# Optimization experiments

Measured on AMD Instinct MI355X. Metric: run time of the kernel, lower is better.

Reference implementation:

```python
import jax, jax.numpy as jnp
import numpy as np

HEADS = 16  # init kwarg 'heads'

def setup_inputs() -> dict:
    key = jax.random.key(0)
    k1, k2, k3 = jax.random.split(key, 3)
    B, S, D = 2, 2048, 1024
    x = jax.random.normal(k1, (B, S, D), dtype=jnp.float32)
    # nn.Linear(dim, 3*dim, bias=False): y = x @ W^T; store as [D, 3D] already transposed.
    w_qkv = jax.random.normal(k2, (D, 3 * D), dtype=jnp.float32) * 0.02
    w_out = jax.random.normal(k3, (D, D), dtype=jnp.float32) * 0.02
    return {"x": x, "w_qkv": w_qkv, "w_out": w_out}

def reference(x, w_qkv, w_out):
    B, S, D = x.shape
    H = HEADS
    hd = D // H
    scale = 1.0 / jnp.sqrt(jnp.asarray(hd, dtype=x.dtype))
    qkv = x @ w_qkv                      # [B, S, 3D]
    q, k, v = jnp.split(qkv, 3, axis=-1)
    def to_heads(t):
        return t.reshape(B, S, H, hd).transpose(0, 2, 1, 3)  # [B, H, S, hd]
    q, k, v = to_heads(q), to_heads(k), to_heads(v)
    scores = jnp.einsum('bhqd,bhkd->bhqk', q, k) * scale      # [B, H, S, S]
    # causal mask: query i attends to keys j <= i
    causal = jnp.tril(jnp.ones((S, S), dtype=bool))
    scores = jnp.where(causal, scores, -jnp.inf)
    p = jax.nn.softmax(scores, axis=-1)  # online-softmax in the original == exact softmax
    o = jnp.einsum('bhqk,bhkd->bhqd', p, v)                   # [B, H, S, hd]
    out = o.transpose(0, 2, 1, 3).reshape(B, S, D)
    return out @ w_out
```

## Files before the change

kernel.cpp:

```cpp
#include <hip/hip_runtime.h>


typedef unsigned short u16;
typedef unsigned int   u32;
typedef __attribute__((ext_vector_type(4))) u16    u16x4;
typedef __attribute__((ext_vector_type(8))) u16    u16x8;
typedef __attribute__((ext_vector_type(4))) short  s16x4;
typedef __attribute__((ext_vector_type(8))) __bf16 bf16x8;
typedef __attribute__((ext_vector_type(4))) float  f32x4;
typedef __attribute__((ext_vector_type(16))) float f32x16;

#define DEV static __device__ __forceinline__

DEV u16 f2b(float f) {
  unsigned u = __float_as_uint(f);
  u += 0x7fffu + ((u >> 16) & 1u);
  return (u16)(u >> 16);
}

DEV void gload_lds16(const void* g, void* l) {
  __builtin_amdgcn_global_load_lds((const __attribute__((address_space(1))) void*)g,
                                   (__attribute__((address_space(3))) void*)l, 16, 0, 0);
}

DEV unsigned lds_off(const void* p) {
  return (unsigned)(unsigned long long)(const __attribute__((address_space(3))) void*)p;
}

DEV s16x4 tr_read(unsigned off) {
  s16x4 d;
  asm volatile("ds_read_b64_tr_b16 %0, %1" : "=v"(d) : "v"(off));
  return d;
}

DEV u32 cvt_pk(float lo, float hi) {
  u32 r;
  asm("v_cvt_pk_bf16_f32 %0, %1, %2" : "=v"(r) : "v"(lo), "v"(hi));
  return r;
}

DEV void pswap(u32& x, u32& y) {
  asm volatile("v_permlane32_swap_b32 %0, %1" : "+v"(x), "+v"(y));
}

DEV f32x4 mfma32(bf16x8 a, bf16x8 b, f32x4 c) {
  return __builtin_amdgcn_mfma_f32_16x16x32_bf16(a, b, c, 0, 0, 0);
}
DEV f32x16 mfma3232(bf16x8 a, bf16x8 b, f32x16 c) {
  return __builtin_amdgcn_mfma_f32_32x32x16_bf16(a, b, c, 0, 0, 0);
}

__global__ __launch_bounds__(256) void prep_kernel(const float* __restrict__ x,
                                                   u16* __restrict__ xb,
                                                   const float* __restrict__ w_qkv,
                                                   u16* __restrict__ wqkvT,
                                                   const float* __restrict__ w_out,
                                                   u16* __restrict__ woutT) {
  __shared__ u16 ls[32][33];
  const int bid = (int)blockIdx.x;
  const int t = threadIdx.x;
  if (bid < 4096) {
    const int i = bid * 256 + t;
    const float4 v = ((const float4*)x)[i];
    u16x4 o = { f2b(v.x), f2b(v.y), f2b(v.z), f2b(v.w) };
    ((u16x4*)xb)[i] = o;
    return;
  }
  const float* w; u16* wt; int Ndim, tn, tk; float s;
  if (bid < 7168) {
    const int q = bid - 4096;
    w = w_qkv; wt = wqkvT; Ndim = 3072;
    tn = (q % 96) * 32; tk = (q / 96) * 32;
    s = (tn < 1024) ? 0.18033688011112042f : 1.0f;
  } else {
    const int q = bid - 7168;
    w = w_out; wt = woutT; Ndim = 1024;
    tn = (q % 32) * 32; tk = (q / 32) * 32;
    s = 1.0f;
  }
  const int r = t >> 3, c4 = (t & 7) * 4;
  const float4 v = *(const float4*)(w + (size_t)(tk + r) * Ndim + tn + c4);
  ls[r][c4 + 0] = f2b(v.x * s); ls[r][c4 + 1] = f2b(v.y * s);
  ls[r][c4 + 2] = f2b(v.z * s); ls[r][c4 + 3] = f2b(v.w * s);
  __syncthreads();
  u16x4 ov = { ls[c4 + 0][r], ls[c4 + 1][r], ls[c4 + 2][r], ls[c4 + 3][r] };
  *(u16x4*)(wt + (size_t)(tn + r) * 1024 + tk + c4) = ov;
}

__global__ __launch_bounds__(512, 2) void gemm_qkv(const u16* __restrict__ A,
                                                   const u16* __restrict__ Bt,
                                                   u16* __restrict__ C, const int ldc) {
  const int gx = gridDim.x;
  const int id = (int)(blockIdx.y * gx + blockIdx.x);
  const int nxp = gx >> 3;
  const int xcd = id & 7, loc = id >> 3;
  const int tn = (xcd * nxp + loc % nxp) * 128;
  const int tm = (loc / nxp) * 128;
  const int tid = (int)threadIdx.x;
  const int lane = tid & 63, wid = tid >> 6;
  const int wm = wid >> 2, wn = wid & 3;
  const int lg = lane >> 4, lc = lane & 15;
  __shared__ __align__(128) u16 lsA[128 * 64];
  __shared__ __align__(128) u16 lsB[128 * 64];

  f32x4 acc[4][2];
#pragma unroll
  for (int i = 0; i < 4; ++i)
#pragma unroll
    for (int j = 0; j < 2; ++j) acc[i][j] = (f32x4){0.f, 0.f, 0.f, 0.f};

  for (int kt = 0; kt < 16; ++kt) {
#pragma unroll
    for (int c = 0; c < 2; ++c) {
      const int p = tid + c * 512;
      const int row = p >> 3, ck = p & 7;
      const int cg = ck ^ (row & 7);
      gload_lds16(A  + (size_t)(tm + row) * 1024 + kt * 64 + cg * 8, (char*)lsA + p * 16);
      gload_lds16(Bt + (size_t)(tn + row) * 1024 + kt * 64 + cg * 8, (char*)lsB + p * 16);
    }
    __syncthreads();
#pragma unroll
    for (int kk = 0; kk < 2; ++kk) {
      bf16x8 af[4], bg[2];
#pragma unroll
      for (int i = 0; i < 4; ++i) {
        const int ar = wm * 64 + i * 16 + lc;
        af[i] = *(const bf16x8*)(lsA + ar * 64 + ((kk * 4 + lg) ^ (ar & 7)) * 8);
      }
#pragma unroll
      for (int j = 0; j < 2; ++j) {
        const int br = wn * 32 + j * 16 + lc;
        bg[j] = *(const bf16x8*)(lsB + br * 64 + ((kk * 4 + lg) ^ (br & 7)) * 8);
      }
#pragma unroll
      for (int i = 0; i < 4; ++i)
#pragma unroll
        for (int j = 0; j < 2; ++j)
          acc[i][j] = mfma32(af[i], bg[j], acc[i][j]);
    }
    __syncthreads();
  }

#pragma unroll
  for (int i = 0; i < 4; ++i) {
#pragma unroll
    for (int r = 0; r < 4; ++r) {
      const int m = tm + wm * 64 + i * 16 + lg * 4 + r;
#pragma unroll
      for (int j = 0; j < 2; ++j) {
        const int n = tn + wn * 32 + j * 16 + lc;
        C[(size_t)m * ldc + n] = f2b(acc[i][j][r]);
      }
    }
  }
}

__global__ __launch_bounds__(256) void gemm_bt64(const u16* __restrict__ A,
                                                 const u16* __restrict__ Bt,
                                                 float* __restrict__ C, const int ldc) {
  const int id = (int)(blockIdx.y * 8 + blockIdx.x);
  const int tn = (id & 7) * 128;
  const int tm = (id >> 3) * 64;
  const int tid = threadIdx.x;
  const int wave = tid >> 6, lane = tid & 63;
  const int wc = wave;
  const int lg = lane >> 4, lc = lane & 15;
  __shared__ __align__(128) u16 lsA[64 * 32];
  __shared__ __align__(128) u16 lsB[128 * 32];

  f32x4 acc[4][2];
#pragma unroll
  for (int i = 0; i < 4; ++i)
#pragma unroll
    for (int j = 0; j < 2; ++j) acc[i][j] = (f32x4){0.f, 0.f, 0.f, 0.f};

  for (int kt = 0; kt < 32; ++kt) {
    {
      const int p = tid;
      const int row = p >> 2, ck = p & 3;
      const int cg = ck ^ ((row >> 1) & 3);
      gload_lds16(A + (size_t)(tm + row) * 1024 + kt * 32 + cg * 8, (char*)lsA + p * 16);
    }
#pragma unroll
    for (int c = 0; c < 2; ++c) {
      const int p = tid + c * 256;
      const int row = p >> 2, ck = p & 3;
      const int cg = ck ^ ((row >> 1) & 3);
      gload_lds16(Bt + (size_t)(tn + row) * 1024 + kt * 32 + cg * 8, (char*)lsB + p * 16);
    }
    __syncthreads();
    bf16x8 af[4], bg[2];
#pragma unroll
    for (int i = 0; i < 4; ++i) {
      const int ar = i * 16 + lc;
      af[i] = *(const bf16x8*)(lsA + ar * 32 + (lg ^ ((ar >> 1) & 3)) * 8);
    }
#pragma unroll
    for (int j = 0; j < 2; ++j) {
      const int br = wc * 32 + j * 16 + lc;
      bg[j] = *(const bf16x8*)(lsB + br * 32 + (lg ^ ((br >> 1) & 3)) * 8);
    }
#pragma unroll
    for (int i = 0; i < 4; ++i)
#pragma unroll
      for (int j = 0; j < 2; ++j)
        acc[i][j] = mfma32(af[i], bg[j], acc[i][j]);
    __syncthreads();
  }

#pragma unroll
  for (int i = 0; i < 4; ++i) {
#pragma unroll
    for (int r = 0; r < 4; ++r) {
      const int m = tm + i * 16 + lg * 4 + r;
#pragma unroll
      for (int j = 0; j < 2; ++j) {
        const int n = tn + wc * 32 + j * 16 + lc;
        C[(size_t)m * ldc + n] = acc[i][j][r];
      }
    }
  }
}

__global__ __launch_bounds__(256, 2) void attn_kernel(const u16* __restrict__ qkv,
                                                      u16* __restrict__ o) {
  const int qb  = 63 - (int)(blockIdx.x >> 5);
  const int bh  = blockIdx.x & 31;
  const int b   = bh >> 4, h = bh & 15;
  const int tid  = threadIdx.x;
  const int wave = tid >> 6, lane = tid & 63;
  const int l31 = lane & 31, lg2 = lane >> 5;

  __shared__ __align__(128) char smem[4][8192];
  __shared__ float lsm[4][32];
  char* wb = smem[wave];
  const unsigned vb = lds_off(wb + 4096);

  const size_t bS = (size_t)b * 2048;
  const int T  = qb + 1;
  const int q0 = qb * 32;

  const u16* qrow = qkv + (bS + q0 + l31) * 3072 + h * 64;
  bf16x8 qf[4];
#pragma unroll
  for (int m = 0; m < 4; ++m)
    qf[m] = *(const bf16x8*)(qrow + 16 * m + 8 * lg2);

  unsigned koff[4], voff[4];
#pragma unroll
  for (int c = 0; c < 4; ++c) {
    const int p = c * 64 + lane;
    {
      const int row = p >> 3;
      const int cg = (p & 7) ^ (row & 7);
      koff[c] = (unsigned)(row * 3072 + 1024 + h * 64 + cg * 8);
    }
    {
      const int s = p >> 3, cw = p & 7;
      voff[c] = (unsigned)((4 * (s >> 2) + (cw >> 1)) * 3072 + 2048 + h * 64
                           + (s & 3) * 16 + (cw & 1) * 8);
    }
  }

  auto STAGE = [&](int t) {
    const u16* base = qkv + (bS + (size_t)t * 32) * 3072;
#pragma unroll
    for (int c = 0; c < 4; ++c)
      gload_lds16(base + koff[c], wb + (c * 64 + lane) * 16);
#pragma unroll
    for (int c = 0; c < 4; ++c)
      gload_lds16(base + voff[c], wb + 4096 + (c * 64 + lane) * 16);
  };

  float lsum = 0.f;
  f32x16 accO[2];
#pragma unroll
  for (int r = 0; r < 16; ++r) { accO[0][r] = 0.f; accO[1][r] = 0.f; }

  if (wave < T) STAGE(wave);

  for (int t = wave; t < T; t += 4) {
    asm volatile("s_waitcnt vmcnt(0)" ::: "memory");
    __builtin_amdgcn_sched_barrier(0);

    const u16* kbp = (const u16*)wb + l31 * 64;
    bf16x8 kf[4];
#pragma unroll
    for (int m = 0; m < 4; ++m)
      kf[m] = *(const bf16x8*)(kbp + (((2 * m + lg2) ^ (l31 & 7)) * 8));
    s16x4 vr[2][2][2];
#pragma unroll
    for (int db = 0; db < 2; ++db)
#pragma unroll
      for (int hh = 0; hh < 2; ++hh) {
        const unsigned a0 = vb +
          (unsigned)(((4 * hh + 2 * lg2) * 4 + db * 2 + (l31 >> 4)) * 128 + (l31 & 15) * 8);
        vr[db][hh][0] = tr_read(a0);
        vr[db][hh][1] = tr_read(a0 + 512);
      }
    asm volatile("s_waitcnt lgkmcnt(0)" ::: "memory");
    __builtin_amdgcn_sched_barrier(0);

    if (t + 4 < T) STAGE(t + 4);
    __builtin_amdgcn_sched_barrier(0);

    f32x16 sc;
#pragma unroll
    for (int r = 0; r < 16; ++r) sc[r] = 0.f;
    __builtin_amdgcn_s_setprio(1);
#pragma unroll
    for (int m = 0; m < 4; ++m)
      sc = mfma3232(kf[m], qf[m], sc);
    __builtin_amdgcn_s_setprio(0);

    float pp[16];
    if (t == T - 1) {
#pragma unroll
      for (int r = 0; r < 16; ++r) {
        const int kvp = (r & 3) + 8 * (r >> 2) + 4 * lg2;
        pp[r] = (kvp <= l31) ? exp2f(sc[r]) : 0.f;
      }
    } else {
#pragma unroll
      for (int r = 0; r < 16; ++r) pp[r] = exp2f(sc[r]);
    }
#pragma unroll
    for (int r = 0; r < 16; ++r) lsum += pp[r];

    u32 a01 = cvt_pk(pp[0], pp[1]),   a23 = cvt_pk(pp[2], pp[3]);
    u32 b01 = cvt_pk(pp[4], pp[5]),   b23 = cvt_pk(pp[6], pp[7]);
    u32 c01 = cvt_pk(pp[8], pp[9]),   c23 = cvt_pk(pp[10], pp[11]);
    u32 d01 = cvt_pk(pp[12], pp[13]), d23 = cvt_pk(pp[14], pp[15]);
    pswap(a01, b01); pswap(a23, b23);
    pswap(c01, d01); pswap(c23, d23);
    union Frag { u32 w[4]; bf16x8 v; };
    Frag f0, f1;
    f0.w[0] = a01; f0.w[1] = a23; f0.w[2] = b01; f0.w[3] = b23;
    f1.w[0] = c01; f1.w[1] = c23; f1.w[2] = d01; f1.w[3] = d23;

    __builtin_amdgcn_s_setprio(1);
#pragma unroll
    for (int db = 0; db < 2; ++db) {
      union { s16x4 hh[2]; bf16x8 v; } u0, u1;
      u0.hh[0] = vr[db][0][0]; u0.hh[1] = vr[db][0][1];
      u1.hh[0] = vr[db][1][0]; u1.hh[1] = vr[db][1][1];
      accO[db] = mfma3232(f0.v, u0.v, accO[db]);
      accO[db] = mfma3232(f1.v, u1.v, accO[db]);
    }
    __builtin_amdgcn_s_setprio(0);
  }

  lsum += __shfl_xor(lsum, 32);
  if (lane < 32) lsm[wave][l31] = lsum;
  float* mA = (float*)smem[0];
  float* mB = (float*)smem[2];
  __syncthreads();
  if ((wave & 1) == 0) {
    float* m = (wave == 0) ? mA : mB;
#pragma unroll
    for (int db = 0; db < 2; ++db)
#pragma unroll
      for (int r = 0; r < 16; ++r) {
        const int qp = (r & 3) + 8 * (r >> 2) + 4 * lg2;
        m[qp * 64 + db * 32 + l31] = accO[db][r];
      }
  }
  __syncthreads();
  if ((wave & 1) == 1) {
    float* m = (wave == 1) ? mA : mB;
#pragma unroll
    for (int db = 0; db < 2; ++db)
#pragma unroll
      for (int r = 0; r < 16; ++r) {
        const int qp = (r & 3) + 8 * (r >> 2) + 4 * lg2;
        m[qp * 64 + db * 32 + l31] += accO[db][r];
      }
  }
  __syncthreads();

  const int q  = tid >> 3;
  const int d0 = (tid & 7) * 8;
  const float inv = 1.f / (lsm[0][q] + lsm[1][q] + lsm[2][q] + lsm[3][q]);
  u16x8 ov;
#pragma unroll
  for (int e = 0; e < 8; ++e)
    ov[e] = f2b((mA[q * 64 + d0 + e] + mB[q * 64 + d0 + e]) * inv);
  *(u16x8*)(o + (bS + q0 + q) * 1024 + h * 64 + d0) = ov;
}

extern "C" void kernel_launch(void* const* d_in, const int* in_sizes, int n_in,
                              void* d_out, int out_size, void* d_ws, size_t ws_size,
                              hipStream_t stream) {
  const float* x     = (const float*)d_in[0];
  const float* w_qkv = (const float*)d_in[1];
  const float* w_out = (const float*)d_in[2];
  float* out = (float*)d_out;
  char* ws = (char*)d_ws;

  u16* xb    = (u16*)(ws + 0);
  u16* wqkvT = (u16*)(ws + 8388608);
  u16* woutT = (u16*)(ws + 14680064);
  u16* qkvb  = (u16*)(ws + 16777216);
  u16* ob    = (u16*)(ws + 41943040);

  prep_kernel<<<8192, 256, 0, stream>>>(x, xb, w_qkv, wqkvT, w_out, woutT);
  gemm_qkv<<<dim3(24, 32), 512, 0, stream>>>(xb, wqkvT, qkvb, 3072);
  attn_kernel<<<2048, 256, 0, stream>>>(qkvb, ob);
  gemm_bt64<<<dim3(8, 64), 256, 0, stream>>>(ob, woutT, out, 1024);
}
```

Baseline: 99.99 us.

## Double-buffer LDS tiles in QKV GEMM with async prefetch and manual waitcnt

The QKV projection GEMM now double-buffers its A/B LDS tiles, issuing the global-to-LDS loads for the next K step before computing on the current one, and waits with explicit vmcnt counts instead of a full syncthreads. It also raises MFMA priority with s_setprio around the matrix ops and changes launch bounds to request 4 blocks per CU. The aim is to hide global load latency behind MFMA work. The cost is twice the LDS per block (64KB), which may limit occupancy below what the new launch bound asks for, and the hand-written waitcnt counts must match the number of outstanding loads exactly.

```diff
diff --git a/kernel.cpp b/kernel.cpp
--- a/kernel.cpp
+++ b/kernel.cpp
@@ -87,7 +87,7 @@
   *(u16x4*)(wt + (size_t)(tn + r) * 1024 + tk + c4) = ov;
 }
 
-__global__ __launch_bounds__(512, 2) void gemm_qkv(const u16* __restrict__ A,
+__global__ __launch_bounds__(512, 4) void gemm_qkv(const u16* __restrict__ A,
                                                    const u16* __restrict__ Bt,
                                                    u16* __restrict__ C, const int ldc) {
   const int gx = gridDim.x;
@@ -100,8 +100,8 @@
   const int lane = tid & 63, wid = tid >> 6;
   const int wm = wid >> 2, wn = wid & 3;
   const int lg = lane >> 4, lc = lane & 15;
-  __shared__ __align__(128) u16 lsA[128 * 64];
-  __shared__ __align__(128) u16 lsB[128 * 64];
+  __shared__ __align__(128) u16 lsA[2][128 * 64];
+  __shared__ __align__(128) u16 lsB[2][128 * 64];
 
   f32x4 acc[4][2];
 #pragma unroll
@@ -109,36 +109,65 @@
 #pragma unroll
     for (int j = 0; j < 2; ++j) acc[i][j] = (f32x4){0.f, 0.f, 0.f, 0.f};
 
+  unsigned asrc[2], bsrc[2], ldst[2];
+#pragma unroll
+  for (int c = 0; c < 2; ++c) {
+    const int p = tid + c * 512;
+    const int row = p >> 3, ck = p & 7;
+    const int cg = ck ^ (row & 7);
+    asrc[c] = (unsigned)((tm + row) * 1024 + cg * 8);
+    bsrc[c] = (unsigned)((tn + row) * 1024 + cg * 8);
+    ldst[c] = (unsigned)(p * 16);
+  }
+
+  auto STAGE = [&](int kt, int bf) {
+    const unsigned ko = (unsigned)(kt * 64);
+#pragma unroll
+    for (int c = 0; c < 2; ++c) {
+      gload_lds16(A  + asrc[c] + ko, (char*)lsA[bf] + ldst[c]);
+      gload_lds16(Bt + bsrc[c] + ko, (char*)lsB[bf] + ldst[c]);
+    }
+  };
+
+  STAGE(0, 0);
+
   for (int kt = 0; kt < 16; ++kt) {
-#pragma unroll
-    for (int c = 0; c < 2; ++c) {
-      const int p = tid + c * 512;
-      const int row = p >> 3, ck = p & 7;
-      const int cg = ck ^ (row & 7);
-      gload_lds16(A  + (size_t)(tm + row) * 1024 + kt * 64 + cg * 8, (char*)lsA + p * 16);
-      gload_lds16(Bt + (size_t)(tn + row) * 1024 + kt * 64 + cg * 8, (char*)lsB + p * 16);
-    }
-    __syncthreads();
+    const int bf = kt & 1;
+    if (kt < 15) {
+      STAGE(kt + 1, bf ^ 1);
+      asm volatile("s_waitcnt vmcnt(4)" ::: "memory");
+    } else {
+      asm volatile("s_waitcnt vmcnt(0)" ::: "memory");
+    }
+    __builtin_amdgcn_sched_barrier(0);
+    __builtin_amdgcn_s_barrier();
+
+    const u16* bA = lsA[bf];
+    const u16* bB = lsB[bf];
 #pragma unroll
     for (int kk = 0; kk < 2; ++kk) {
       bf16x8 af[4], bg[2];
 #pragma unroll
       for (int i = 0; i < 4; ++i) {
         const int ar = wm * 64 + i * 16 + lc;
-        af[i] = *(const bf16x8*)(lsA + ar * 64 + ((kk * 4 + lg) ^ (ar & 7)) * 8);
+        af[i] = *(const bf16x8*)(bA + ar * 64 + ((kk * 4 + lg) ^ (ar & 7)) * 8);
       }
 #pragma unroll
       for (int j = 0; j < 2; ++j) {
         const int br = wn * 32 + j * 16 + lc;
-        bg[j] = *(const bf16x8*)(lsB + br * 64 + ((kk * 4 + lg) ^ (br & 7)) * 8);
-      }
+        bg[j] = *(const bf16x8*)(bB + br * 64 + ((kk * 4 + lg) ^ (br & 7)) * 8);
+      }
+      __builtin_amdgcn_s_setprio(1);
 #pragma unroll
       for (int i = 0; i < 4; ++i)
 #pragma unroll
         for (int j = 0; j < 2; ++j)
           acc[i][j] = mfma32(af[i], bg[j], acc[i][j]);
-    }
-    __syncthreads();
+      __builtin_amdgcn_s_setprio(0);
+    }
+    asm volatile("s_waitcnt lgkmcnt(0)" ::: "memory");
+    __builtin_amdgcn_sched_barrier(0);
+    __builtin_amdgcn_s_barrier();
   }
 
 #pragma unroll
```

Result: no change. 101.8 us (+1.8%).

## Fuse fp32-to-bf16 conversion of x into QKV GEMM tile loads

Applied to the files above, without the earlier changes.

Drops the separate pass that converts x to bf16 in the prep kernel. The QKV GEMM now loads fp32 x directly into registers, converts it with packed bf16 instructions and writes it into swizzled LDS, while B keeps using direct global-to-LDS loads. This removes a full write and read of the bf16 copy of x plus half the prep blocks. In exchange, each x tile is read from global memory at twice the byte size and by 24 column blocks, and the A load now goes through registers without asynchronous LDS loading.

```diff
diff --git a/kernel.cpp b/kernel.cpp
--- a/kernel.cpp
+++ b/kernel.cpp
@@ -5,6 +5,7 @@
 typedef unsigned int   u32;
 typedef __attribute__((ext_vector_type(4))) u16    u16x4;
 typedef __attribute__((ext_vector_type(8))) u16    u16x8;
+typedef __attribute__((ext_vector_type(4))) u32    u32x4;
 typedef __attribute__((ext_vector_type(4))) short  s16x4;
 typedef __attribute__((ext_vector_type(8))) __bf16 bf16x8;
 typedef __attribute__((ext_vector_type(4))) float  f32x4;
@@ -50,30 +51,20 @@
   return __builtin_amdgcn_mfma_f32_32x32x16_bf16(a, b, c, 0, 0, 0);
 }
 
-__global__ __launch_bounds__(256) void prep_kernel(const float* __restrict__ x,
-                                                   u16* __restrict__ xb,
-                                                   const float* __restrict__ w_qkv,
+__global__ __launch_bounds__(256) void prep_kernel(const float* __restrict__ w_qkv,
                                                    u16* __restrict__ wqkvT,
                                                    const float* __restrict__ w_out,
                                                    u16* __restrict__ woutT) {
   __shared__ u16 ls[32][33];
   const int bid = (int)blockIdx.x;
   const int t = threadIdx.x;
-  if (bid < 4096) {
-    const int i = bid * 256 + t;
-    const float4 v = ((const float4*)x)[i];
-    u16x4 o = { f2b(v.x), f2b(v.y), f2b(v.z), f2b(v.w) };
-    ((u16x4*)xb)[i] = o;
-    return;
-  }
   const float* w; u16* wt; int Ndim, tn, tk; float s;
-  if (bid < 7168) {
-    const int q = bid - 4096;
+  if (bid < 3072) {
     w = w_qkv; wt = wqkvT; Ndim = 3072;
-    tn = (q % 96) * 32; tk = (q / 96) * 32;
+    tn = (bid % 96) * 32; tk = (bid / 96) * 32;
     s = (tn < 1024) ? 0.18033688011112042f : 1.0f;
   } else {
-    const int q = bid - 7168;
+    const int q = bid - 3072;
     w = w_out; wt = woutT; Ndim = 1024;
     tn = (q % 32) * 32; tk = (q / 32) * 32;
     s = 1.0f;
@@ -87,7 +78,7 @@
   *(u16x4*)(wt + (size_t)(tn + r) * 1024 + tk + c4) = ov;
 }
 
-__global__ __launch_bounds__(512, 2) void gemm_qkv(const u16* __restrict__ A,
+__global__ __launch_bounds__(512, 2) void gemm_qkv(const float* __restrict__ X,
                                                    const u16* __restrict__ Bt,
                                                    u16* __restrict__ C, const int ldc) {
   const int gx = gridDim.x;
@@ -109,14 +100,35 @@
 #pragma unroll
     for (int j = 0; j < 2; ++j) acc[i][j] = (f32x4){0.f, 0.f, 0.f, 0.f};
 
+  unsigned asrc[2], bsrc[2], ldst[2];
+#pragma unroll
+  for (int c = 0; c < 2; ++c) {
+    const int p = tid + c * 512;
+    const int row = p >> 3;
+    const int cg = (p & 7) ^ (row & 7);
+    asrc[c] = (unsigned)((tm + row) * 1024 + cg * 8);
+    bsrc[c] = (unsigned)((tn + row) * 1024 + cg * 8);
+    ldst[c] = (unsigned)(p * 16);
+  }
+
   for (int kt = 0; kt < 16; ++kt) {
+    const unsigned ko = (unsigned)(kt * 64);
+    f32x4 a0[2], a1[2];
 #pragma unroll
     for (int c = 0; c < 2; ++c) {
-      const int p = tid + c * 512;
-      const int row = p >> 3, ck = p & 7;
-      const int cg = ck ^ (row & 7);
-      gload_lds16(A  + (size_t)(tm + row) * 1024 + kt * 64 + cg * 8, (char*)lsA + p * 16);
-      gload_lds16(Bt + (size_t)(tn + row) * 1024 + kt * 64 + cg * 8, (char*)lsB + p * 16);
+      const float* ap = X + asrc[c] + ko;
+      a0[c] = *(const f32x4*)ap;
+      a1[c] = *(const f32x4*)(ap + 4);
+      gload_lds16(Bt + bsrc[c] + ko, (char*)lsB + ldst[c]);
+    }
+#pragma unroll
+    for (int c = 0; c < 2; ++c) {
+      u32x4 w;
+      w[0] = cvt_pk(a0[c][0], a0[c][1]);
+      w[1] = cvt_pk(a0[c][2], a0[c][3]);
+      w[2] = cvt_pk(a1[c][0], a1[c][1]);
+      w[3] = cvt_pk(a1[c][2], a1[c][3]);
+      *(u32x4*)((char*)lsA + ldst[c]) = w;
     }
     __syncthreads();
 #pragma unroll
@@ -397,14 +409,13 @@
   float* out = (float*)d_out;
   char* ws = (char*)d_ws;
 
-  u16* xb    = (u16*)(ws + 0);
   u16* wqkvT = (u16*)(ws + 8388608);
   u16* woutT = (u16*)(ws + 14680064);
   u16* qkvb  = (u16*)(ws + 16777216);
   u16* ob    = (u16*)(ws + 41943040);
 
-  prep_kernel<<<8192, 256, 0, stream>>>(x, xb, w_qkv, wqkvT, w_out, woutT);
-  gemm_qkv<<<dim3(24, 32), 512, 0, stream>>>(xb, wqkvT, qkvb, 3072);
+  prep_kernel<<<4096, 256, 0, stream>>>(w_qkv, wqkvT, w_out, woutT);
+  gemm_qkv<<<dim3(24, 32), 512, 0, stream>>>(x, wqkvT, qkvb, 3072);
   attn_kernel<<<2048, 256, 0, stream>>>(qkvb, ob);
   gemm_bt64<<<dim3(8, 64), 256, 0, stream>>>(ob, woutT, out, 1024);
 }
```

Result: slower. 102.7 us (+2.8%).
